# Kernel optimization log

Hardware: AMD Instinct MI355X
Metric: run time of the kernel (lower is better)

The kernel has to match this reference:

```python
import jax, jax.numpy as jnp
import numpy as np

A, S, D, V = 128, 512, 768, 30522
NL, LW = 10, 5  # n label categories, words per category
MASK_ID = 103
NEG = -1e30


def setup_inputs() -> dict:
    key = jax.random.key(0)
    ks = jax.random.split(key, 12)
    scale = 0.02
    input_ids = jax.random.randint(ks[0], (A, S), 0, 30000)
    input_ids = jnp.where(input_ids == MASK_ID, MASK_ID + 1, input_ids)  # strip accidental masks
    mask_pos = jax.random.randint(ks[1], (A,), 1, 3)  # one [MASK] per row, before position 3
    input_ids = input_ids.at[jnp.arange(A), mask_pos].set(MASK_ID)
    length = jax.random.randint(ks[2], (A,), 1, 400)
    bert_out = jax.random.normal(ks[3], (A, S, D), jnp.float32)
    label_words = jax.random.randint(ks[4], (NL, LW), 0, V)
    return {
        "bert_out": bert_out,
        "input_ids": input_ids,
        "length": length,
        "label_words": label_words,
        "W_senti": jax.random.normal(ks[5], (2, D), jnp.float32) * scale,
        "b_senti": jnp.zeros((2,), jnp.float32),
        "W_dense": jax.random.normal(ks[6], (D, 2 * D), jnp.float32) * scale,
        "b_dense": jnp.zeros((D,), jnp.float32),
        "W_prob": jax.random.normal(ks[7], (V, D), jnp.float32) * scale,
        "b_prob": jnp.zeros((V,), jnp.float32),
        "W_lab": jax.random.normal(ks[8], (NL, 2, LW), jnp.float32) * scale,
    }


def reference(bert_out, input_ids, length, label_words,
              W_senti, b_senti, W_dense, b_dense, W_prob, b_prob, W_lab):
    a, s, d = bert_out.shape
    # pooler = [CLS] hidden state -> senti head (dropout is identity in eval)
    senti_out = bert_out[:, 0] @ W_senti.T + b_senti  # [A,2]

    # gather the (single) [MASK] token hidden state per sample
    mask_pos = jnp.argmax(input_ids == MASK_ID, axis=1)        # [A]
    mask_logit = bert_out[jnp.arange(a), mask_pos]             # [A,D]

    # ragged attention pool over bert_out[i, 3:3+length[i]] vectorized via masking
    pos = jnp.arange(s)
    valid = (pos[None, :] >= 3) & (pos[None, :] < 3 + length[:, None])  # [A,S]
    scores = jnp.einsum('asd,ad->as', bert_out, mask_logit)
    scores = jnp.where(valid, scores, NEG)
    w = jax.nn.softmax(scores, axis=1)                         # [A,S]
    att = jnp.einsum('as,asd->ad', w, bert_out)                # [A,D]

    x = jnp.concatenate([att, mask_logit], axis=-1)            # [A,2D]
    h = jnp.tanh(x @ W_dense.T + b_dense)                      # [A,D]
    p = jnp.tanh(h @ W_prob.T + b_prob)                        # [A,V]

    # per-category label-word gather + small no-bias linear, stacked on dim 2
    lp = p[:, label_words]                                     # [A,NL,LW]
    out = jnp.einsum('alw,lkw->akl', lp, W_lab)                # [A,2,NL]
    return senti_out, out
```

## Files before the change

kernel.cpp:

```cpp
#include <hip/hip_runtime.h>
#include <stdint.h>

#define A_ 128
#define S_ 512
#define D_ 768
#define C_ 16
#define MASKID 103

typedef short bf16x8_t __attribute__((ext_vector_type(8)));
typedef float floatx4_t __attribute__((ext_vector_type(4)));

__device__ __forceinline__ unsigned short f2bf(float f) {
    union { unsigned int u; float f; } v; v.f = f;
    unsigned int u = v.u;
    return (unsigned short)((u + 0x7fffu + ((u >> 16) & 1u)) >> 16);
}

__global__ __launch_bounds__(256) void attn_part(
    const float* __restrict__ bert,
    const int* __restrict__ ids,
    const int* __restrict__ length,
    const int* __restrict__ label_words,
    const float* __restrict__ W_prob,
    const float* __restrict__ b_prob,
    const float* __restrict__ W_dense,
    const float* __restrict__ W_senti,
    const float* __restrict__ b_senti,
    unsigned short* __restrict__ ws_Wpw,
    float* __restrict__ ws_bp,
    unsigned short* __restrict__ ws_Wd,
    unsigned short* __restrict__ ws_x,
    float* __restrict__ part_m,
    float* __restrict__ part_l,
    float* __restrict__ part_acc,
    float* __restrict__ d_out)
{
    int bx = blockIdx.x;
    int tid = threadIdx.x;
    if (bx >= A_ * C_) {
        int r = bx - A_ * C_;
        if (r < 50) {
            int word = label_words[r];
            const float* src = W_prob + (size_t)word * D_;
            for (int j = tid; j < D_; j += 256) ws_Wpw[r * D_ + j] = f2bf(src[j]);
            if (tid == 0) ws_bp[r] = b_prob[word];
        } else {
            for (int j = tid; j < D_; j += 256) ws_Wpw[r * D_ + j] = 0;
            if (tid == 0) ws_bp[r] = 0.f;
        }
        const float4* src4 = (const float4*)(W_dense + (size_t)r * 18432);
        ushort4* dst4 = (ushort4*)(ws_Wd + (size_t)r * 18432);
#pragma unroll
        for (int it = 0; it < 18; it++) {
            float4 v = src4[tid + 256 * it];
            ushort4 o;
            o.x = f2bf(v.x); o.y = f2bf(v.y); o.z = f2bf(v.z); o.w = f2bf(v.w);
            dst4[tid + 256 * it] = o;
        }
        return;
    }
    int a = bx >> 4, c = bx & 15;
    int wave = tid >> 6, lane = tid & 63;
    int d0 = lane * 4;

    __shared__ int s_minpos;
    __shared__ float red_m[4], red_l[4];
    __shared__ float red_acc[4][D_];

    const float* base = bert + (size_t)a * S_ * D_;

    if (c == 1 && wave == 0) {
        const float* q = base + d0;
        float4 v0 = *(const float4*)(q);
        float4 v1 = *(const float4*)(q + 256);
        float4 v2 = *(const float4*)(q + 512);
        float4 u0 = *(const float4*)(W_senti + d0);
        float4 u1 = *(const float4*)(W_senti + d0 + 256);
        float4 u2 = *(const float4*)(W_senti + d0 + 512);
        float4 t0 = *(const float4*)(W_senti + D_ + d0);
        float4 t1 = *(const float4*)(W_senti + D_ + d0 + 256);
        float4 t2 = *(const float4*)(W_senti + D_ + d0 + 512);
        float rv[12], w0[12], w1[12];
        rv[0]=v0.x; rv[1]=v0.y; rv[2]=v0.z; rv[3]=v0.w;
        rv[4]=v1.x; rv[5]=v1.y; rv[6]=v1.z; rv[7]=v1.w;
        rv[8]=v2.x; rv[9]=v2.y; rv[10]=v2.z; rv[11]=v2.w;
        w0[0]=u0.x; w0[1]=u0.y; w0[2]=u0.z; w0[3]=u0.w;
        w0[4]=u1.x; w0[5]=u1.y; w0[6]=u1.z; w0[7]=u1.w;
        w0[8]=u2.x; w0[9]=u2.y; w0[10]=u2.z; w0[11]=u2.w;
        w1[0]=t0.x; w1[1]=t0.y; w1[2]=t0.z; w1[3]=t0.w;
        w1[4]=t1.x; w1[5]=t1.y; w1[6]=t1.z; w1[7]=t1.w;
        w1[8]=t2.x; w1[9]=t2.y; w1[10]=t2.z; w1[11]=t2.w;
        float p0 = 0.f, p1 = 0.f;
#pragma unroll
        for (int k = 0; k < 12; k++) { p0 = fmaf(rv[k], w0[k], p0); p1 = fmaf(rv[k], w1[k], p1); }
#pragma unroll
        for (int off = 32; off >= 1; off >>= 1) {
            p0 += __shfl_xor(p0, off, 64);
            p1 += __shfl_xor(p1, off, 64);
        }
        if (lane == 0) {
            d_out[a * 2 + 0] = p0 + b_senti[0];
            d_out[a * 2 + 1] = p1 + b_senti[1];
        }
    }

    if (tid == 0) s_minpos = S_;
    __syncthreads();
    for (int p = tid; p < S_; p += 256)
        if (ids[a * S_ + p] == MASKID) atomicMin(&s_minpos, p);
    __syncthreads();
    int mp = (s_minpos >= S_) ? 0 : s_minpos;

    float ml[12];
    {
        const float* q = base + (size_t)mp * D_ + d0;
        float4 v0 = *(const float4*)(q);
        float4 v1 = *(const float4*)(q + 256);
        float4 v2 = *(const float4*)(q + 512);
        ml[0]=v0.x; ml[1]=v0.y; ml[2]=v0.z; ml[3]=v0.w;
        ml[4]=v1.x; ml[5]=v1.y; ml[6]=v1.z; ml[7]=v1.w;
        ml[8]=v2.x; ml[9]=v2.y; ml[10]=v2.z; ml[11]=v2.w;
    }
    if (c == 0 && wave == 0) {
#pragma unroll
        for (int j = 0; j < 3; j++) {
            ushort4 o;
            o.x = f2bf(ml[4*j]);   o.y = f2bf(ml[4*j+1]);
            o.z = f2bf(ml[4*j+2]); o.w = f2bf(ml[4*j+3]);
            *(ushort4*)(ws_x + (size_t)a * 1536 + D_ + d0 + 256 * j) = o;
        }
    }
    int len = length[a]; if (len > S_ - 3) len = S_ - 3;

    float m = -3.0e38f, l = 0.f;
    float acc[12];
#pragma unroll
    for (int k = 0; k < 12; k++) acc[k] = 0.f;

    int v = c + 16 * wave;
    for (; v + 64 < len; v += 128) {
        const float* qa = base + (size_t)(3 + v) * D_ + d0;
        const float* qb = base + (size_t)(3 + v + 64) * D_ + d0;
        float4 a0 = *(const float4*)(qa);
        float4 a1 = *(const float4*)(qa + 256);
        float4 a2 = *(const float4*)(qa + 512);
        float4 b0 = *(const float4*)(qb);
        float4 b1 = *(const float4*)(qb + 256);
        float4 b2 = *(const float4*)(qb + 512);
        float ra[12], rb[12];
        ra[0]=a0.x; ra[1]=a0.y; ra[2]=a0.z; ra[3]=a0.w;
        ra[4]=a1.x; ra[5]=a1.y; ra[6]=a1.z; ra[7]=a1.w;
        ra[8]=a2.x; ra[9]=a2.y; ra[10]=a2.z; ra[11]=a2.w;
        rb[0]=b0.x; rb[1]=b0.y; rb[2]=b0.z; rb[3]=b0.w;
        rb[4]=b1.x; rb[5]=b1.y; rb[6]=b1.z; rb[7]=b1.w;
        rb[8]=b2.x; rb[9]=b2.y; rb[10]=b2.z; rb[11]=b2.w;
        float pa = 0.f, pb = 0.f;
#pragma unroll
        for (int k = 0; k < 12; k++) { pa = fmaf(ra[k], ml[k], pa); pb = fmaf(rb[k], ml[k], pb); }
#pragma unroll
        for (int off = 32; off >= 1; off >>= 1) {
            pa += __shfl_xor(pa, off, 64);
            pb += __shfl_xor(pb, off, 64);
        }
        float mn = fmaxf(m, fmaxf(pa, pb));
        float alpha = __expf(m - mn);
        float wa = __expf(pa - mn);
        float wb = __expf(pb - mn);
        l = l * alpha + wa + wb;
#pragma unroll
        for (int k = 0; k < 12; k++)
            acc[k] = fmaf(acc[k], alpha, fmaf(wa, ra[k], wb * rb[k]));
        m = mn;
    }
    for (; v < len; v += 64) {
        const float* qa = base + (size_t)(3 + v) * D_ + d0;
        float4 a0 = *(const float4*)(qa);
        float4 a1 = *(const float4*)(qa + 256);
        float4 a2 = *(const float4*)(qa + 512);
        float ra[12];
        ra[0]=a0.x; ra[1]=a0.y; ra[2]=a0.z; ra[3]=a0.w;
        ra[4]=a1.x; ra[5]=a1.y; ra[6]=a1.z; ra[7]=a1.w;
        ra[8]=a2.x; ra[9]=a2.y; ra[10]=a2.z; ra[11]=a2.w;
        float pa = 0.f;
#pragma unroll
        for (int k = 0; k < 12; k++) pa = fmaf(ra[k], ml[k], pa);
#pragma unroll
        for (int off = 32; off >= 1; off >>= 1)
            pa += __shfl_xor(pa, off, 64);
        float mn = fmaxf(m, pa);
        float alpha = __expf(m - mn);
        float wa = __expf(pa - mn);
        l = l * alpha + wa;
#pragma unroll
        for (int k = 0; k < 12; k++) acc[k] = fmaf(acc[k], alpha, wa * ra[k]);
        m = mn;
    }
    if (lane == 0) { red_m[wave] = m; red_l[wave] = l; }
#pragma unroll
    for (int j = 0; j < 3; j++) {
        floatx4_t t = { acc[4*j], acc[4*j+1], acc[4*j+2], acc[4*j+3] };
        *(floatx4_t*)&red_acc[wave][d0 + 256 * j] = t;
    }
    __syncthreads();

    float m0 = red_m[0], m1 = red_m[1], m2 = red_m[2], m3 = red_m[3];
    float M = fmaxf(fmaxf(m0, m1), fmaxf(m2, m3));
    float f0 = __expf(m0 - M), f1 = __expf(m1 - M);
    float f2 = __expf(m2 - M), f3 = __expf(m3 - M);
    int pc = (a * C_ + c) * D_;
#pragma unroll
    for (int e = 0; e < 3; e++) {
        int d = tid + 256 * e;
        part_acc[pc + d] = f0 * red_acc[0][d] + f1 * red_acc[1][d]
                         + f2 * red_acc[2][d] + f3 * red_acc[3][d];
    }
    if (tid == 0) {
        part_m[a * C_ + c] = M;
        part_l[a * C_ + c] = f0 * red_l[0] + f1 * red_l[1] + f2 * red_l[2] + f3 * red_l[3];
    }
}

__global__ __launch_bounds__(256) void merge_kernel(
    const float* __restrict__ part_m,
    const float* __restrict__ part_l,
    const float* __restrict__ part_acc,
    unsigned short* __restrict__ ws_x)
{
    int a = blockIdx.x, tid = threadIdx.x;
    float mc[C_], lc[C_];
#pragma unroll
    for (int c = 0; c < C_; c++) { mc[c] = part_m[a * C_ + c]; lc[c] = part_l[a * C_ + c]; }
    float M = mc[0];
#pragma unroll
    for (int c = 1; c < C_; c++) M = fmaxf(M, mc[c]);
    float fac[C_]; float denom = 0.f;
#pragma unroll
    for (int c = 0; c < C_; c++) { fac[c] = __expf(mc[c] - M); denom += fac[c] * lc[c]; }
    float inv = 1.0f / fmaxf(denom, 1e-30f);

    const float* pa = part_acc + (size_t)a * C_ * D_;
#pragma unroll
    for (int e = 0; e < 3; e++) {
        int d = tid + 256 * e;
        float s = 0.f;
#pragma unroll
        for (int c = 0; c < C_; c++) s = fmaf(fac[c], pa[c * D_ + d], s);
        ws_x[(size_t)a * 1536 + d] = f2bf(s * inv);
    }
}

__global__ __launch_bounds__(256) void dense_kernel(
    const unsigned short* __restrict__ ws_x,
    const unsigned short* __restrict__ ws_Wd,
    const float* __restrict__ b_dense,
    unsigned short* __restrict__ ws_h)
{
    int tid = threadIdx.x;
    int wave = tid >> 6, lane = tid & 63;
    int r = lane & 15, q = lane >> 4;
    int T = blockIdx.x;
    int m_t = T / 48, n_t = T % 48;
    const bf16x8_t* Ap = (const bf16x8_t*)(ws_x  + (size_t)(m_t * 16 + r) * 1536 + wave * 384 + q * 8);
    const bf16x8_t* Bp = (const bf16x8_t*)(ws_Wd + (size_t)(n_t * 16 + r) * 1536 + wave * 384 + q * 8);
    floatx4_t acc = {0.f, 0.f, 0.f, 0.f};
#pragma unroll
    for (int kk = 0; kk < 12; kk++)
        acc = __builtin_amdgcn_mfma_f32_16x16x32_bf16(Ap[kk * 4], Bp[kk * 4], acc, 0, 0, 0);
    __shared__ float part[4][256];
#pragma unroll
    for (int reg = 0; reg < 4; reg++)
        part[wave][(q * 4 + reg) * 16 + r] = acc[reg];
    __syncthreads();
    float sum = part[0][tid] + part[1][tid] + part[2][tid] + part[3][tid];
    int row = tid >> 4, col = tid & 15;
    int n = n_t * 16 + col;
    float h = tanhf(sum + b_dense[n]);
    ws_h[(size_t)(m_t * 16 + row) * D_ + n] = f2bf(h);
}

__global__ __launch_bounds__(256) void label_kernel(
    const unsigned short* __restrict__ ws_h,
    const unsigned short* __restrict__ ws_Wpw,
    const float* __restrict__ ws_bp,
    const float* __restrict__ W_lab,
    float* __restrict__ d_out)
{
    int tid = threadIdx.x;
    int wave = tid >> 6, lane = tid & 63;
    int r = lane & 15, q = lane >> 4;
    int m_t = blockIdx.x;
    int n_t = wave;
    const bf16x8_t* Ap = (const bf16x8_t*)(ws_h + (size_t)(m_t * 16 + r) * 768 + q * 8);
    const bf16x8_t* Bp = (const bf16x8_t*)(ws_Wpw + (size_t)(n_t * 16 + r) * 768 + q * 8);
    floatx4_t acc = {0.f, 0.f, 0.f, 0.f};
#pragma unroll
    for (int kk = 0; kk < 24; kk++)
        acc = __builtin_amdgcn_mfma_f32_16x16x32_bf16(Ap[kk * 4], Bp[kk * 4], acc, 0, 0, 0);
    __shared__ float lp_s[16][64];
    int col = n_t * 16 + r;
    float bp = ws_bp[col];
#pragma unroll
    for (int reg = 0; reg < 4; reg++)
        lp_s[q * 4 + reg][col] = tanhf(acc[reg] + bp);
    __syncthreads();
    for (int t = tid; t < 320; t += 256) {
        int al = t / 20, rem = t % 20;
        int k = rem / 10, lb = rem % 10;
        float s = 0.f;
#pragma unroll
        for (int w = 0; w < 5; w++)
            s = fmaf(lp_s[al][lb * 5 + w], W_lab[(lb * 2 + k) * 5 + w], s);
        d_out[256 + (m_t * 16 + al) * 20 + rem] = s;
    }
}

extern "C" void kernel_launch(void* const* d_in, const int* in_sizes, int n_in,
                              void* d_out, int out_size, void* d_ws, size_t ws_size,
                              hipStream_t stream) {
    const float* bert    = (const float*)d_in[0];
    const int* ids       = (const int*)d_in[1];
    const int* length    = (const int*)d_in[2];
    const int* label_words = (const int*)d_in[3];
    const float* W_senti = (const float*)d_in[4];
    const float* b_senti = (const float*)d_in[5];
    const float* W_dense = (const float*)d_in[6];
    const float* b_dense = (const float*)d_in[7];
    const float* W_prob  = (const float*)d_in[8];
    const float* b_prob  = (const float*)d_in[9];
    const float* W_lab   = (const float*)d_in[10];
    float* out = (float*)d_out;

    char* ws = (char*)d_ws;
    unsigned short* ws_x   = (unsigned short*)(ws + 0);
    unsigned short* ws_h   = (unsigned short*)(ws + 393216);
    unsigned short* ws_Wpw = (unsigned short*)(ws + 589824);
    float*          ws_bp  = (float*)(ws + 688128);
    unsigned short* ws_Wd  = (unsigned short*)(ws + 688384);
    float*          part_m = (float*)(ws + 3047680);
    float*          part_l = (float*)(ws + 3055872);
    float*        part_acc = (float*)(ws + 3064064);

    attn_part<<<A_ * C_ + 64, 256, 0, stream>>>(bert, ids, length, label_words,
        W_prob, b_prob, W_dense, W_senti, b_senti,
        ws_Wpw, ws_bp, ws_Wd, ws_x, part_m, part_l, part_acc, out);
    merge_kernel<<<A_, 256, 0, stream>>>(part_m, part_l, part_acc, ws_x);
    dense_kernel<<<384, 256, 0, stream>>>(ws_x, ws_Wd, b_dense, ws_h);
    label_kernel<<<8, 256, 0, stream>>>(ws_h, ws_Wpw, ws_bp, W_lab, out);
}
```

Before: 323.7 us.

## Fuse merge and label stages via last-block atomic counters

Drops the separate merge and label kernels. The last attention block to finish for each sample, found with an atomic counter, now does the softmax-partial merge. The last dense block for each 16-row tile runs the label-word GEMM and W_lab projection. This removes two kernel launches and their inter-kernel gaps, at the cost of a memset, threadfences and atomics, plus serialized tail work inside the final blocks.

```diff
diff --git a/kernel.cpp b/kernel.cpp
--- a/kernel.cpp
+++ b/kernel.cpp
@@ -33,6 +33,7 @@
     float* __restrict__ part_m,
     float* __restrict__ part_l,
     float* __restrict__ part_acc,
+    int* __restrict__ cnt_a,
     float* __restrict__ d_out)
 {
     int bx = blockIdx.x;
@@ -64,6 +65,7 @@
     int d0 = lane * 4;
 
     __shared__ int s_minpos;
+    __shared__ int s_last;
     __shared__ float red_m[4], red_l[4];
     __shared__ float red_acc[4][D_];
 
@@ -218,34 +220,35 @@
         part_m[a * C_ + c] = M;
         part_l[a * C_ + c] = f0 * red_l[0] + f1 * red_l[1] + f2 * red_l[2] + f3 * red_l[3];
     }
-}
-
-__global__ __launch_bounds__(256) void merge_kernel(
-    const float* __restrict__ part_m,
-    const float* __restrict__ part_l,
-    const float* __restrict__ part_acc,
-    unsigned short* __restrict__ ws_x)
-{
-    int a = blockIdx.x, tid = threadIdx.x;
-    float mc[C_], lc[C_];
-#pragma unroll
-    for (int c = 0; c < C_; c++) { mc[c] = part_m[a * C_ + c]; lc[c] = part_l[a * C_ + c]; }
-    float M = mc[0];
-#pragma unroll
-    for (int c = 1; c < C_; c++) M = fmaxf(M, mc[c]);
-    float fac[C_]; float denom = 0.f;
-#pragma unroll
-    for (int c = 0; c < C_; c++) { fac[c] = __expf(mc[c] - M); denom += fac[c] * lc[c]; }
-    float inv = 1.0f / fmaxf(denom, 1e-30f);
-
-    const float* pa = part_acc + (size_t)a * C_ * D_;
-#pragma unroll
-    for (int e = 0; e < 3; e++) {
-        int d = tid + 256 * e;
-        float s = 0.f;
-#pragma unroll
-        for (int c = 0; c < C_; c++) s = fmaf(fac[c], pa[c * D_ + d], s);
-        ws_x[(size_t)a * 1536 + d] = f2bf(s * inv);
+
+    __threadfence();
+    __syncthreads();
+    if (tid == 0) s_last = atomicAdd(&cnt_a[a], 1);
+    __syncthreads();
+    if (s_last == C_ - 1) {
+        __threadfence();
+        float mc[C_], lc[C_];
+#pragma unroll
+        for (int c2 = 0; c2 < C_; c2++) {
+            mc[c2] = part_m[a * C_ + c2];
+            lc[c2] = part_l[a * C_ + c2];
+        }
+        float M2 = mc[0];
+#pragma unroll
+        for (int c2 = 1; c2 < C_; c2++) M2 = fmaxf(M2, mc[c2]);
+        float fac[C_]; float denom = 0.f;
+#pragma unroll
+        for (int c2 = 0; c2 < C_; c2++) { fac[c2] = __expf(mc[c2] - M2); denom += fac[c2] * lc[c2]; }
+        float inv = 1.0f / fmaxf(denom, 1e-30f);
+        const float* pa2 = part_acc + (size_t)a * C_ * D_;
+#pragma unroll
+        for (int e = 0; e < 3; e++) {
+            int d = tid + 256 * e;
+            float s = 0.f;
+#pragma unroll
+            for (int c2 = 0; c2 < C_; c2++) s = fmaf(fac[c2], pa2[c2 * D_ + d], s);
+            ws_x[(size_t)a * 1536 + d] = f2bf(s * inv);
+        }
     }
 }
 
@@ -253,7 +256,12 @@
     const unsigned short* __restrict__ ws_x,
     const unsigned short* __restrict__ ws_Wd,
     const float* __restrict__ b_dense,
-    unsigned short* __restrict__ ws_h)
+    unsigned short* __restrict__ ws_h,
+    const unsigned short* __restrict__ ws_Wpw,
+    const float* __restrict__ ws_bp,
+    const float* __restrict__ W_lab,
+    int* __restrict__ cnt_d,
+    float* __restrict__ d_out)
 {
     int tid = threadIdx.x;
     int wave = tid >> 6, lane = tid & 63;
@@ -267,6 +275,7 @@
     for (int kk = 0; kk < 12; kk++)
         acc = __builtin_amdgcn_mfma_f32_16x16x32_bf16(Ap[kk * 4], Bp[kk * 4], acc, 0, 0, 0);
     __shared__ float part[4][256];
+    __shared__ int s_last;
 #pragma unroll
     for (int reg = 0; reg < 4; reg++)
         part[wave][(q * 4 + reg) * 16 + r] = acc[reg];
@@ -276,41 +285,36 @@
     int n = n_t * 16 + col;
     float h = tanhf(sum + b_dense[n]);
     ws_h[(size_t)(m_t * 16 + row) * D_ + n] = f2bf(h);
-}
-
-__global__ __launch_bounds__(256) void label_kernel(
-    const unsigned short* __restrict__ ws_h,
-    const unsigned short* __restrict__ ws_Wpw,
-    const float* __restrict__ ws_bp,
-    const float* __restrict__ W_lab,
-    float* __restrict__ d_out)
-{
-    int tid = threadIdx.x;
-    int wave = tid >> 6, lane = tid & 63;
-    int r = lane & 15, q = lane >> 4;
-    int m_t = blockIdx.x;
-    int n_t = wave;
-    const bf16x8_t* Ap = (const bf16x8_t*)(ws_h + (size_t)(m_t * 16 + r) * 768 + q * 8);
-    const bf16x8_t* Bp = (const bf16x8_t*)(ws_Wpw + (size_t)(n_t * 16 + r) * 768 + q * 8);
-    floatx4_t acc = {0.f, 0.f, 0.f, 0.f};
-#pragma unroll
-    for (int kk = 0; kk < 24; kk++)
-        acc = __builtin_amdgcn_mfma_f32_16x16x32_bf16(Ap[kk * 4], Bp[kk * 4], acc, 0, 0, 0);
-    __shared__ float lp_s[16][64];
-    int col = n_t * 16 + r;
-    float bp = ws_bp[col];
-#pragma unroll
-    for (int reg = 0; reg < 4; reg++)
-        lp_s[q * 4 + reg][col] = tanhf(acc[reg] + bp);
-    __syncthreads();
-    for (int t = tid; t < 320; t += 256) {
-        int al = t / 20, rem = t % 20;
-        int k = rem / 10, lb = rem % 10;
-        float s = 0.f;
-#pragma unroll
-        for (int w = 0; w < 5; w++)
-            s = fmaf(lp_s[al][lb * 5 + w], W_lab[(lb * 2 + k) * 5 + w], s);
-        d_out[256 + (m_t * 16 + al) * 20 + rem] = s;
+
+    __threadfence();
+    __syncthreads();
+    if (tid == 0) s_last = atomicAdd(&cnt_d[m_t], 1);
+    __syncthreads();
+    if (s_last == 47) {
+        __threadfence();
+        int n_t2 = wave;
+        const bf16x8_t* Ap2 = (const bf16x8_t*)(ws_h + (size_t)(m_t * 16 + r) * 768 + q * 8);
+        const bf16x8_t* Bp2 = (const bf16x8_t*)(ws_Wpw + (size_t)(n_t2 * 16 + r) * 768 + q * 8);
+        floatx4_t acc2 = {0.f, 0.f, 0.f, 0.f};
+#pragma unroll
+        for (int kk = 0; kk < 24; kk++)
+            acc2 = __builtin_amdgcn_mfma_f32_16x16x32_bf16(Ap2[kk * 4], Bp2[kk * 4], acc2, 0, 0, 0);
+        __shared__ float lp_s[16][64];
+        int col2 = n_t2 * 16 + r;
+        float bp = ws_bp[col2];
+#pragma unroll
+        for (int reg = 0; reg < 4; reg++)
+            lp_s[q * 4 + reg][col2] = tanhf(acc2[reg] + bp);
+        __syncthreads();
+        for (int t = tid; t < 320; t += 256) {
+            int al = t / 20, rem = t % 20;
+            int k = rem / 10, lb = rem % 10;
+            float s = 0.f;
+#pragma unroll
+            for (int w = 0; w < 5; w++)
+                s = fmaf(lp_s[al][lb * 5 + w], W_lab[(lb * 2 + k) * 5 + w], s);
+            d_out[256 + (m_t * 16 + al) * 20 + rem] = s;
+        }
     }
 }
 
@@ -339,11 +343,13 @@
     float*          part_m = (float*)(ws + 3047680);
     float*          part_l = (float*)(ws + 3055872);
     float*        part_acc = (float*)(ws + 3064064);
-
+    int*            cnt_a  = (int*)(ws + 9355520);
+    int*            cnt_d  = (int*)(ws + 9356032);
+
+    hipMemsetAsync(ws + 9355520, 0, 1024, stream);
     attn_part<<<A_ * C_ + 64, 256, 0, stream>>>(bert, ids, length, label_words,
         W_prob, b_prob, W_dense, W_senti, b_senti,
-        ws_Wpw, ws_bp, ws_Wd, ws_x, part_m, part_l, part_acc, out);
-    merge_kernel<<<A_, 256, 0, stream>>>(part_m, part_l, part_acc, ws_x);
-    dense_kernel<<<384, 256, 0, stream>>>(ws_x, ws_Wd, b_dense, ws_h);
-    label_kernel<<<8, 256, 0, stream>>>(ws_h, ws_Wpw, ws_bp, W_lab, out);
+        ws_Wpw, ws_bp, ws_Wd, ws_x, part_m, part_l, part_acc, cnt_a, out);
+    dense_kernel<<<384, 256, 0, stream>>>(ws_x, ws_Wd, b_dense, ws_h,
+        ws_Wpw, ws_bp, W_lab, cnt_d, out);
 }
```

Result: slower. 735.6 us (+127.3%).
